# Kernel optimization log

Measured on AMD Instinct MI355X. Metric: run time of the kernel, lower is better.

## Reference

```python
import jax, jax.numpy as jnp
import numpy as np

B, N, DIN, DOUT = 32, 1024, 256, 256


def setup_inputs() -> dict:
    key = jax.random.key(0)
    ks = jax.random.split(key, 7)
    s = 1.0 / np.sqrt(DIN)
    return {
        "x": jax.random.normal(ks[0], (B, N, DIN), dtype=jnp.float32),
        "Wq": jax.random.uniform(ks[1], (DOUT, DIN), minval=-s, maxval=s, dtype=jnp.float32),
        "bq": jax.random.uniform(ks[2], (DOUT,), minval=-s, maxval=s, dtype=jnp.float32),
        "Wk": jax.random.uniform(ks[3], (DOUT, DIN), minval=-s, maxval=s, dtype=jnp.float32),
        "bk": jax.random.uniform(ks[4], (DOUT,), minval=-s, maxval=s, dtype=jnp.float32),
        "Wv": jax.random.uniform(ks[5], (DOUT, DIN), minval=-s, maxval=s, dtype=jnp.float32),
        "bv": jax.random.uniform(ks[6], (DOUT,), minval=-s, maxval=s, dtype=jnp.float32),
    }


def reference(x, Wq, bq, Wk, bk, Wv, bv):
    # q, k, v: (B, N, Dout)
    q = jnp.einsum("bnd,od->bno", x, Wq) + bq
    k = jnp.einsum("bnd,od->bno", x, Wk) + bk
    v = jnp.einsum("bnd,od->bno", x, Wv) + bv
    # logits: (B, N, N) = q @ k^T per batch
    logits = jnp.einsum("bnd,bmd->bnm", q, k)
    # NOTE: softmax over the BATCH dim (axis=0), as in the original module
    attn = jax.nn.softmax(logits, axis=0)
    out = jnp.einsum("bnm,bmd->bnd", attn, v)  # (B, N, Dout)
    return out
```

## Files before the change

### kernel.cpp

```cpp
#include <hip/hip_runtime.h>

typedef __bf16 bf16x8 __attribute__((ext_vector_type(8)));
typedef __bf16 bf16x4 __attribute__((ext_vector_type(4)));
typedef float  f32x4  __attribute__((ext_vector_type(4)));

#define BM 128
#define BN 128
#define BK 64

__device__ __forceinline__ void g2l16(const void* g, void* l) {
    __builtin_amdgcn_global_load_lds((const __attribute__((address_space(1))) void*)g,
                                     (__attribute__((address_space(3))) void*)l, 16, 0, 0);
}

template<int EPI>
__global__ __launch_bounds__(256)
void gemm_nt(const __bf16* __restrict__ A, const __bf16* __restrict__ B,
             void* __restrict__ Cv, const float* __restrict__ bias,
             int lda, int ldb, int ldc, int K,
             long sA, long sB, long sC)
{
    __shared__ __align__(16) char smem[36864];
    __bf16* As = (__bf16*)smem;
    __bf16* Bs = (__bf16*)(smem + 16384);

    const int tid  = threadIdx.x;
    const int w    = tid >> 6;
    const int lane = tid & 63;
    const int quad = lane >> 4;
    const int l16  = lane & 15;
    const int wm   = w & 1;
    const int wn   = w >> 1;

    const int m0 = blockIdx.x * BM;
    const int n0 = blockIdx.y * BN;
    const int z  = blockIdx.z;

    const __bf16* Ab = A + (size_t)z * sA;
    const __bf16* Bb = B + (size_t)z * sB;

    const int srow = (w << 3) + (lane >> 3);
    const int scol = ((lane & 7) ^ (lane >> 3)) << 3;
    char* ldsA = (char*)As + (size_t)w * 1024;
    char* ldsB = (char*)Bs + (size_t)w * 1024;

    const __bf16* Ag = Ab + (size_t)(m0 + srow) * lda + scol;
    const __bf16* Bg = Bb + (size_t)(n0 + srow) * ldb + scol;

    f32x4 acc[4][4] = {};

    for (int k0 = 0; k0 < K; k0 += BK) {
        __syncthreads();
        #pragma unroll
        for (int c = 0; c < 4; c++)
            g2l16(Ag + (size_t)(c * 32) * lda + k0, ldsA + c * 4096);
        #pragma unroll
        for (int c = 0; c < 4; c++)
            g2l16(Bg + (size_t)(c * 32) * ldb + k0, ldsB + c * 4096);
        __syncthreads();

        #pragma unroll
        for (int kk = 0; kk < BK; kk += 32) {
            const int ub = kk >> 3;
            bf16x8 a[4], b[4];
            #pragma unroll
            for (int mt = 0; mt < 4; mt++) {
                const int row = wm * 64 + mt * 16 + l16;
                const int cp  = ((quad + ub) ^ (row & 7)) << 3;
                a[mt] = *(const bf16x8*)&As[row * BK + cp];
            }
            #pragma unroll
            for (int nt = 0; nt < 4; nt++) {
                const int row = wn * 64 + nt * 16 + l16;
                const int cp  = ((quad + ub) ^ (row & 7)) << 3;
                b[nt] = *(const bf16x8*)&Bs[row * BK + cp];
            }
            #pragma unroll
            for (int mt = 0; mt < 4; mt++)
                #pragma unroll
                for (int nt = 0; nt < 4; nt++)
                    acc[mt][nt] = __builtin_amdgcn_mfma_f32_16x16x32_bf16(
                        a[mt], b[nt], acc[mt][nt], 0, 0, 0);
        }
    }

    __syncthreads();

    if constexpr (EPI == 2 || EPI == 4) {
        __bf16* eb = (__bf16*)smem;
        const bool tr = (EPI == 4) && (z == 2);
        if (!tr) {
            float bn[4];
            if constexpr (EPI == 4) {
                #pragma unroll
                for (int nt = 0; nt < 4; nt++)
                    bn[nt] = bias[z * 256 + n0 + wn * 64 + nt * 16 + l16];
            }
            #pragma unroll
            for (int mt = 0; mt < 4; mt++) {
                const int row = wm * 64 + mt * 16 + quad * 4;
                #pragma unroll
                for (int nt = 0; nt < 4; nt++) {
                    const int col = wn * 64 + nt * 16 + l16;
                    #pragma unroll
                    for (int r = 0; r < 4; r++) {
                        float v = acc[mt][nt][r];
                        if constexpr (EPI == 2) v = __expf(v);
                        else                    v += bn[nt];
                        eb[(row + r) * 144 + col] = (__bf16)v;
                    }
                }
            }
        } else {
            #pragma unroll
            for (int nt = 0; nt < 4; nt++) {
                const float bn = bias[z * 256 + n0 + wn * 64 + nt * 16 + l16];
                const int erow = wn * 64 + nt * 16 + l16;
                #pragma unroll
                for (int mt = 0; mt < 4; mt++) {
                    bf16x4 pk;
                    #pragma unroll
                    for (int r = 0; r < 4; r++) pk[r] = (__bf16)(acc[mt][nt][r] + bn);
                    *(bf16x4*)&eb[erow * 144 + wm * 64 + mt * 16 + quad * 4] = pk;
                }
            }
        }
        __syncthreads();
        const int row = tid >> 1, seg = tid & 1;
        __bf16* dst;
        if (!tr) {
            dst = (__bf16*)Cv + (size_t)z * sC + (size_t)(m0 + row) * ldc + n0 + seg * 64;
        } else {
            dst = (__bf16*)Cv + 2 * sC + (size_t)(m0 >> 10) * 262144
                + (size_t)(n0 + row) * 1024 + (m0 & 1023) + seg * 64;
        }
        #pragma unroll
        for (int u = 0; u < 8; u++)
            *(bf16x8*)(dst + u * 8) = *(const bf16x8*)&eb[row * 144 + seg * 64 + u * 8];
    } else {
        float* ef = (float*)smem;
        float* C  = (float*)Cv + (size_t)z * sC;
        #pragma unroll
        for (int h = 0; h < 2; h++) {
            if (h) __syncthreads();
            if (wm == h) {
                #pragma unroll
                for (int mt = 0; mt < 4; mt++) {
                    const int row = mt * 16 + quad * 4;
                    #pragma unroll
                    for (int nt = 0; nt < 4; nt++) {
                        const int col = wn * 64 + nt * 16 + l16;
                        #pragma unroll
                        for (int r = 0; r < 4; r++)
                            ef[(row + r) * 132 + col] = acc[mt][nt][r];
                    }
                }
            }
            __syncthreads();
            const int row = tid >> 2, seg = tid & 3;
            float* dst = C + (size_t)(m0 + h * 64 + row) * ldc + n0 + seg * 32;
            #pragma unroll
            for (int u = 0; u < 8; u++)
                *(f32x4*)(dst + u * 4) = *(const f32x4*)&ef[row * 132 + seg * 32 + u * 4];
        }
    }
}

__global__ __launch_bounds__(256)
void cvt_all(const float* __restrict__ x,
             const float* __restrict__ Wq, const float* __restrict__ Wk,
             const float* __restrict__ Wv,
             const float* __restrict__ bq, const float* __restrict__ bk,
             const float* __restrict__ bv,
             __bf16* __restrict__ xb, __bf16* __restrict__ Wqb,
             float* __restrict__ bpack)
{
    const int i = blockIdx.x * 256 + threadIdx.x;
    if (i < 1073152) {
        const float* s; __bf16* d; int off;
        if (i < 1048576)      { s = x;  d = xb;            off = i; }
        else if (i < 1056768) { s = Wq; d = Wqb;           off = i - 1048576; }
        else if (i < 1064960) { s = Wk; d = Wqb + 131072;  off = i - 1056768; }
        else                  { s = Wv; d = Wqb + 262144;  off = i - 1064960; }
        const float4* s4 = (const float4*)s;
        const float4 f0 = s4[off * 2], f1 = s4[off * 2 + 1];
        bf16x8 o;
        o[0] = (__bf16)f0.x; o[1] = (__bf16)f0.y; o[2] = (__bf16)f0.z; o[3] = (__bf16)f0.w;
        o[4] = (__bf16)f1.x; o[5] = (__bf16)f1.y; o[6] = (__bf16)f1.z; o[7] = (__bf16)f1.w;
        ((bf16x8*)d)[off] = o;
    } else if (i < 1073344) {
        const int j = i - 1073152;
        const int sel = j >> 6, jj = j & 63;
        const float* s = sel == 0 ? bq : (sel == 1 ? bk : bv);
        ((float4*)bpack)[j] = ((const float4*)s)[jj];
    }
}

__global__ __launch_bounds__(256)
void softmax_norm(__bf16* __restrict__ E)
{
    const size_t p = (size_t)blockIdx.x * 256 + threadIdx.x;
    bf16x8* E8 = (bf16x8*)E;
    bf16x8 e[32];
    #pragma unroll
    for (int b = 0; b < 32; b++) e[b] = E8[(size_t)b * 131072 + p];
    float s[8] = {0.f, 0.f, 0.f, 0.f, 0.f, 0.f, 0.f, 0.f};
    #pragma unroll
    for (int b = 0; b < 32; b++)
        #pragma unroll
        for (int j = 0; j < 8; j++) s[j] += (float)e[b][j];
    float rs[8];
    #pragma unroll
    for (int j = 0; j < 8; j++) rs[j] = 1.0f / s[j];
    #pragma unroll
    for (int b = 0; b < 32; b++) {
        bf16x8 o = e[b];
        #pragma unroll
        for (int j = 0; j < 8; j++) o[j] = (__bf16)((float)o[j] * rs[j]);
        E8[(size_t)b * 131072 + p] = o;
    }
}

extern "C" void kernel_launch(void* const* d_in, const int* in_sizes, int n_in,
                              void* d_out, int out_size, void* d_ws, size_t ws_size,
                              hipStream_t stream)
{
    const float* x  = (const float*)d_in[0];
    const float* Wq = (const float*)d_in[1];
    const float* bq = (const float*)d_in[2];
    const float* Wk = (const float*)d_in[3];
    const float* bk = (const float*)d_in[4];
    const float* Wv = (const float*)d_in[5];
    const float* bv = (const float*)d_in[6];
    float* out = (float*)d_out;

    char* ws = (char*)d_ws;
    __bf16* xb    = (__bf16*)(ws);
    __bf16* qkv   = (__bf16*)(ws + (16u << 20));
    __bf16* E     = (__bf16*)(ws + (64u << 20));
    __bf16* Wqb   = (__bf16*)(ws + (128u << 20));
    float*  bpack = (float*) (ws + (128u << 20) + (3u << 18));

    cvt_all<<<4194, 256, 0, stream>>>(x, Wq, Wk, Wv, bq, bk, bv, xb, Wqb, bpack);

    gemm_nt<4><<<dim3(256, 2, 3), 256, 0, stream>>>(xb, Wqb, qkv, bpack,
                                                    256, 256, 256, 256,
                                                    0, 131072, 8388608);

    gemm_nt<2><<<dim3(8, 8, 32), 256, 0, stream>>>(qkv, qkv + 8388608, E, nullptr,
                                                   256, 256, 1024, 256,
                                                   262144, 262144, 1048576);

    softmax_norm<<<512, 256, 0, stream>>>(E);

    gemm_nt<3><<<dim3(8, 2, 32), 256, 0, stream>>>(E, qkv + 2 * 8388608, out, nullptr,
                                                   1024, 1024, 256, 1024,
                                                   1048576, 262144, 262144);
}
```

Measured before the change: 232.8 us.

## Fuse softmax normalization into PV GEMM A-load and flatten batch-major grid

The softmax pass no longer rewrites E. It only computes per-position reciprocal sums over the batch and stores them as fp32. A new PV GEMM scales E by those reciprocals while staging the A tile into LDS, so one full read-write pass over the 64MB E buffer is gone. The QK GEMM now uses a flat grid with batch as the fastest index, so the 32 batches of the same tile run together, which may help the later cross-batch reduction hit L2. Epilogues now write registers straight to global memory instead of going through LDS, which risks less-coalesced stores. The PV A-tile is also loaded with plain register loads instead of async LDS loads, and it reads extra fp32 scale data.

Result: faster. 213.5 us (-8.3%).

```diff
diff --git a/kernel.cpp b/kernel.cpp
--- a/kernel.cpp
+++ b/kernel.cpp
@@ -13,16 +13,15 @@
                                      (__attribute__((address_space(3))) void*)l, 16, 0, 0);
 }
 
-template<int EPI>
+template<int EPI, int FLAT>
 __global__ __launch_bounds__(256)
 void gemm_nt(const __bf16* __restrict__ A, const __bf16* __restrict__ B,
              void* __restrict__ Cv, const float* __restrict__ bias,
              int lda, int ldb, int ldc, int K,
              long sA, long sB, long sC)
 {
-    __shared__ __align__(16) char smem[36864];
-    __bf16* As = (__bf16*)smem;
-    __bf16* Bs = (__bf16*)(smem + 16384);
+    __shared__ __align__(16) __bf16 As[BM * BK];
+    __shared__ __align__(16) __bf16 Bs[BN * BK];
 
     const int tid  = threadIdx.x;
     const int w    = tid >> 6;
@@ -32,9 +31,18 @@
     const int wm   = w & 1;
     const int wn   = w >> 1;
 
-    const int m0 = blockIdx.x * BM;
-    const int n0 = blockIdx.y * BN;
-    const int z  = blockIdx.z;
+    int m0, n0, z;
+    if constexpr (FLAT) {
+        const int id = blockIdx.x;
+        z = id & 31;
+        const int xy = id >> 5;
+        m0 = (xy & 7) * BM;
+        n0 = (xy >> 3) * BN;
+    } else {
+        m0 = blockIdx.x * BM;
+        n0 = blockIdx.y * BN;
+        z  = blockIdx.z;
+    }
 
     const __bf16* Ab = A + (size_t)z * sA;
     const __bf16* Bb = B + (size_t)z * sB;
@@ -84,84 +92,134 @@
         }
     }
 
-    __syncthreads();
-
-    if constexpr (EPI == 2 || EPI == 4) {
-        __bf16* eb = (__bf16*)smem;
-        const bool tr = (EPI == 4) && (z == 2);
-        if (!tr) {
-            float bn[4];
-            if constexpr (EPI == 4) {
+    #pragma unroll
+    for (int mt = 0; mt < 4; mt++) {
+        const int mb = m0 + wm * 64 + mt * 16 + quad * 4;
+        #pragma unroll
+        for (int nt = 0; nt < 4; nt++) {
+            const int n = n0 + wn * 64 + nt * 16 + l16;
+            if constexpr (EPI == 2) {
+                __bf16* C = (__bf16*)Cv + (size_t)z * sC;
                 #pragma unroll
-                for (int nt = 0; nt < 4; nt++)
-                    bn[nt] = bias[z * 256 + n0 + wn * 64 + nt * 16 + l16];
-            }
-            #pragma unroll
-            for (int mt = 0; mt < 4; mt++) {
-                const int row = wm * 64 + mt * 16 + quad * 4;
-                #pragma unroll
-                for (int nt = 0; nt < 4; nt++) {
-                    const int col = wn * 64 + nt * 16 + l16;
+                for (int r = 0; r < 4; r++)
+                    C[(size_t)(mb + r) * ldc + n] = (__bf16)__expf(acc[mt][nt][r]);
+            } else {
+                const float bn = bias[z * 256 + n];
+                if (z < 2) {
+                    __bf16* C = (__bf16*)Cv + (size_t)z * sC;
                     #pragma unroll
-                    for (int r = 0; r < 4; r++) {
-                        float v = acc[mt][nt][r];
-                        if constexpr (EPI == 2) v = __expf(v);
-                        else                    v += bn[nt];
-                        eb[(row + r) * 144 + col] = (__bf16)v;
-                    }
-                }
-            }
-        } else {
-            #pragma unroll
-            for (int nt = 0; nt < 4; nt++) {
-                const float bn = bias[z * 256 + n0 + wn * 64 + nt * 16 + l16];
-                const int erow = wn * 64 + nt * 16 + l16;
-                #pragma unroll
-                for (int mt = 0; mt < 4; mt++) {
+                    for (int r = 0; r < 4; r++)
+                        C[(size_t)(mb + r) * ldc + n] = (__bf16)(acc[mt][nt][r] + bn);
+                } else {
+                    __bf16* C = (__bf16*)Cv + 2 * sC;
+                    const int bidx = mb >> 10, mloc = mb & 1023;
                     bf16x4 pk;
                     #pragma unroll
                     for (int r = 0; r < 4; r++) pk[r] = (__bf16)(acc[mt][nt][r] + bn);
-                    *(bf16x4*)&eb[erow * 144 + wm * 64 + mt * 16 + quad * 4] = pk;
+                    *(bf16x4*)(C + (size_t)bidx * 262144 + (size_t)n * 1024 + mloc) = pk;
                 }
             }
         }
+    }
+}
+
+__global__ __launch_bounds__(256)
+void gemm_pv(const __bf16* __restrict__ E, const float* __restrict__ Srcp,
+             const __bf16* __restrict__ vT, float* __restrict__ out)
+{
+    __shared__ __align__(16) __bf16 As[128 * 64];
+    __shared__ __align__(16) __bf16 Bs[128 * 64];
+
+    const int tid  = threadIdx.x;
+    const int w    = tid >> 6;
+    const int lane = tid & 63;
+    const int quad = lane >> 4;
+    const int l16  = lane & 15;
+    const int wm   = w & 1;
+    const int wn   = w >> 1;
+
+    const int id = blockIdx.x;
+    const int z  = id & 31;
+    const int xy = id >> 5;
+    const int m0 = (xy & 7) * 128;
+    const int n0 = (xy >> 3) * 128;
+
+    const __bf16* Eb = E  + (size_t)z * 1048576;
+    const __bf16* Vb = vT + (size_t)z * 262144;
+    float*        Ob = out + (size_t)z * 262144;
+
+    const int srow = (w << 3) + (lane >> 3);
+    const int scol = ((lane & 7) ^ (lane >> 3)) << 3;
+    char* ldsB = (char*)Bs + (size_t)w * 1024;
+    const __bf16* Bg = Vb + (size_t)(n0 + srow) * 1024 + scol;
+
+    const int arow = tid >> 1;
+    const int auh  = (tid & 1) * 4;
+    const __bf16* Ag = Eb + (size_t)(m0 + arow) * 1024;
+    const float*  Sg = Srcp + (size_t)(m0 + arow) * 1024;
+    __bf16* Ad = As + arow * 64;
+
+    f32x4 acc[4][4] = {};
+
+    for (int k0 = 0; k0 < 1024; k0 += BK) {
         __syncthreads();
-        const int row = tid >> 1, seg = tid & 1;
-        __bf16* dst;
-        if (!tr) {
-            dst = (__bf16*)Cv + (size_t)z * sC + (size_t)(m0 + row) * ldc + n0 + seg * 64;
-        } else {
-            dst = (__bf16*)Cv + 2 * sC + (size_t)(m0 >> 10) * 262144
-                + (size_t)(n0 + row) * 1024 + (m0 & 1023) + seg * 64;
-        }
-        #pragma unroll
-        for (int u = 0; u < 8; u++)
-            *(bf16x8*)(dst + u * 8) = *(const bf16x8*)&eb[row * 144 + seg * 64 + u * 8];
-    } else {
-        float* ef = (float*)smem;
-        float* C  = (float*)Cv + (size_t)z * sC;
-        #pragma unroll
-        for (int h = 0; h < 2; h++) {
-            if (h) __syncthreads();
-            if (wm == h) {
+        #pragma unroll
+        for (int c = 0; c < 4; c++)
+            g2l16(Bg + (size_t)(c * 32) * 1024 + k0, ldsB + c * 4096);
+        #pragma unroll
+        for (int s = 0; s < 4; s++) {
+            const int u   = auh + s;
+            const int col = k0 + u * 8;
+            bf16x8 e  = *(const bf16x8*)(Ag + col);
+            f32x4  r0 = *(const f32x4*)(Sg + col);
+            f32x4  r1 = *(const f32x4*)(Sg + col + 4);
+            bf16x8 en;
+            en[0] = (__bf16)((float)e[0] * r0[0]);
+            en[1] = (__bf16)((float)e[1] * r0[1]);
+            en[2] = (__bf16)((float)e[2] * r0[2]);
+            en[3] = (__bf16)((float)e[3] * r0[3]);
+            en[4] = (__bf16)((float)e[4] * r1[0]);
+            en[5] = (__bf16)((float)e[5] * r1[1]);
+            en[6] = (__bf16)((float)e[6] * r1[2]);
+            en[7] = (__bf16)((float)e[7] * r1[3]);
+            *(bf16x8*)(Ad + ((u ^ (arow & 7)) << 3)) = en;
+        }
+        __syncthreads();
+
+        #pragma unroll
+        for (int kk = 0; kk < BK; kk += 32) {
+            const int ub = kk >> 3;
+            bf16x8 a[4], b[4];
+            #pragma unroll
+            for (int mt = 0; mt < 4; mt++) {
+                const int row = wm * 64 + mt * 16 + l16;
+                const int cp  = ((quad + ub) ^ (row & 7)) << 3;
+                a[mt] = *(const bf16x8*)&As[row * BK + cp];
+            }
+            #pragma unroll
+            for (int nt = 0; nt < 4; nt++) {
+                const int row = wn * 64 + nt * 16 + l16;
+                const int cp  = ((quad + ub) ^ (row & 7)) << 3;
+                b[nt] = *(const bf16x8*)&Bs[row * BK + cp];
+            }
+            #pragma unroll
+            for (int mt = 0; mt < 4; mt++)
                 #pragma unroll
-                for (int mt = 0; mt < 4; mt++) {
-                    const int row = mt * 16 + quad * 4;
-                    #pragma unroll
-                    for (int nt = 0; nt < 4; nt++) {
-                        const int col = wn * 64 + nt * 16 + l16;
-                        #pragma unroll
-                        for (int r = 0; r < 4; r++)
-                            ef[(row + r) * 132 + col] = acc[mt][nt][r];
-                    }
-                }
-            }
-            __syncthreads();
-            const int row = tid >> 2, seg = tid & 3;
-            float* dst = C + (size_t)(m0 + h * 64 + row) * ldc + n0 + seg * 32;
-            #pragma unroll
-            for (int u = 0; u < 8; u++)
-                *(f32x4*)(dst + u * 4) = *(const f32x4*)&ef[row * 132 + seg * 32 + u * 4];
+                for (int nt = 0; nt < 4; nt++)
+                    acc[mt][nt] = __builtin_amdgcn_mfma_f32_16x16x32_bf16(
+                        a[mt], b[nt], acc[mt][nt], 0, 0, 0);
+        }
+    }
+
+    #pragma unroll
+    for (int mt = 0; mt < 4; mt++) {
+        const int mb = m0 + wm * 64 + mt * 16 + quad * 4;
+        #pragma unroll
+        for (int nt = 0; nt < 4; nt++) {
+            const int n = n0 + wn * 64 + nt * 16 + l16;
+            #pragma unroll
+            for (int r = 0; r < 4; r++)
+                Ob[(size_t)(mb + r) * 256 + n] = acc[mt][nt][r];
         }
     }
 }
@@ -197,28 +255,24 @@
 }
 
 __global__ __launch_bounds__(256)
-void softmax_norm(__bf16* __restrict__ E)
+void reduce_s(const __bf16* __restrict__ E, float* __restrict__ Srcp)
 {
     const size_t p = (size_t)blockIdx.x * 256 + threadIdx.x;
-    bf16x8* E8 = (bf16x8*)E;
-    bf16x8 e[32];
-    #pragma unroll
-    for (int b = 0; b < 32; b++) e[b] = E8[(size_t)b * 131072 + p];
+    const bf16x8* E8 = (const bf16x8*)E;
     float s[8] = {0.f, 0.f, 0.f, 0.f, 0.f, 0.f, 0.f, 0.f};
     #pragma unroll
-    for (int b = 0; b < 32; b++)
-        #pragma unroll
-        for (int j = 0; j < 8; j++) s[j] += (float)e[b][j];
-    float rs[8];
-    #pragma unroll
-    for (int j = 0; j < 8; j++) rs[j] = 1.0f / s[j];
-    #pragma unroll
     for (int b = 0; b < 32; b++) {
-        bf16x8 o = e[b];
-        #pragma unroll
-        for (int j = 0; j < 8; j++) o[j] = (__bf16)((float)o[j] * rs[j]);
-        E8[(size_t)b * 131072 + p] = o;
-    }
+        bf16x8 e = E8[(size_t)b * 131072 + p];
+        #pragma unroll
+        for (int j = 0; j < 8; j++) s[j] += (float)e[j];
+    }
+    f32x4 r0, r1;
+    #pragma unroll
+    for (int j = 0; j < 4; j++) r0[j] = __builtin_amdgcn_rcpf(s[j]);
+    #pragma unroll
+    for (int j = 0; j < 4; j++) r1[j] = __builtin_amdgcn_rcpf(s[j + 4]);
+    ((f32x4*)Srcp)[p * 2]     = r0;
+    ((f32x4*)Srcp)[p * 2 + 1] = r1;
 }
 
 extern "C" void kernel_launch(void* const* d_in, const int* in_sizes, int n_in,
@@ -235,6 +289,7 @@
     float* out = (float*)d_out;
 
     char* ws = (char*)d_ws;
+    float*  Srcp  = (float*) (ws);
     __bf16* xb    = (__bf16*)(ws);
     __bf16* qkv   = (__bf16*)(ws + (16u << 20));
     __bf16* E     = (__bf16*)(ws + (64u << 20));
@@ -243,17 +298,15 @@
 
     cvt_all<<<4194, 256, 0, stream>>>(x, Wq, Wk, Wv, bq, bk, bv, xb, Wqb, bpack);
 
-    gemm_nt<4><<<dim3(256, 2, 3), 256, 0, stream>>>(xb, Wqb, qkv, bpack,
-                                                    256, 256, 256, 256,
-                                                    0, 131072, 8388608);
-
-    gemm_nt<2><<<dim3(8, 8, 32), 256, 0, stream>>>(qkv, qkv + 8388608, E, nullptr,
-                                                   256, 256, 1024, 256,
-                                                   262144, 262144, 1048576);
-
-    softmax_norm<<<512, 256, 0, stream>>>(E);
-
-    gemm_nt<3><<<dim3(8, 2, 32), 256, 0, stream>>>(E, qkv + 2 * 8388608, out, nullptr,
-                                                   1024, 1024, 256, 1024,
-                                                   1048576, 262144, 262144);
-}
+    gemm_nt<4, 0><<<dim3(256, 2, 3), 256, 0, stream>>>(xb, Wqb, qkv, bpack,
+                                                       256, 256, 256, 256,
+                                                       0, 131072, 8388608);
+
+    gemm_nt<2, 1><<<2048, 256, 0, stream>>>(qkv, qkv + 8388608, E, nullptr,
+                                            256, 256, 1024, 256,
+                                            262144, 262144, 1048576);
+
+    reduce_s<<<512, 256, 0, stream>>>(E, Srcp);
+
+    gemm_pv<<<512, 256, 0, stream>>>(E, Srcp, qkv + 2 * 8388608, out);
+}
```

## Split GEMM into specialized kernels with transposed tiles, direct epilogue stores, batch-interleaved grid

Applied to the files above, without the earlier changes.

Replaces the templated GEMM with three specialized kernels that share a core loop. Each kernel computes transposed output tiles (e.g. W·xᵀ, k·qᵀ), so the MFMA accumulator layout maps to contiguous 4-element stores, and the LDS staging epilogue and its extra barriers are dropped. V is written into a new vT layout with the batch interleaved, which lets the PV GEMM run as 64x128 tiles and doubles its block count. Block indices are remapped so adjacent blocks handle different batches, which may spread memory traffic. The direct stores are narrower (8 bytes for bf16) than the previous 16-byte coalesced stores, which risks lower store efficiency. The softmax reciprocal also switches to the hardware rcp.

Result: faster. 203.8 us (-12.4%).

```diff
diff --git a/kernel.cpp b/kernel.cpp
--- a/kernel.cpp
+++ b/kernel.cpp
@@ -4,164 +4,181 @@
 typedef __bf16 bf16x4 __attribute__((ext_vector_type(4)));
 typedef float  f32x4  __attribute__((ext_vector_type(4)));
 
-#define BM 128
-#define BN 128
-#define BK 64
-
 __device__ __forceinline__ void g2l16(const void* g, void* l) {
     __builtin_amdgcn_global_load_lds((const __attribute__((address_space(1))) void*)g,
                                      (__attribute__((address_space(3))) void*)l, 16, 0, 0);
 }
 
-template<int EPI>
-__global__ __launch_bounds__(256)
-void gemm_nt(const __bf16* __restrict__ A, const __bf16* __restrict__ B,
-             void* __restrict__ Cv, const float* __restrict__ bias,
-             int lda, int ldb, int ldc, int K,
-             long sA, long sB, long sC)
-{
-    __shared__ __align__(16) char smem[36864];
-    __bf16* As = (__bf16*)smem;
-    __bf16* Bs = (__bf16*)(smem + 16384);
-
-    const int tid  = threadIdx.x;
-    const int w    = tid >> 6;
-    const int lane = tid & 63;
-    const int quad = lane >> 4;
-    const int l16  = lane & 15;
-    const int wm   = w & 1;
-    const int wn   = w >> 1;
-
-    const int m0 = blockIdx.x * BM;
-    const int n0 = blockIdx.y * BN;
-    const int z  = blockIdx.z;
-
-    const __bf16* Ab = A + (size_t)z * sA;
-    const __bf16* Bb = B + (size_t)z * sB;
+template<int MCH, int NCH>
+__device__ __forceinline__ void gemm_core(
+    const __bf16* __restrict__ At, const __bf16* __restrict__ Bt,
+    int lda, int ldb, int K,
+    __bf16* As, __bf16* Bs, f32x4 (&acc)[MCH][NCH], int tid)
+{
+    const int w = tid >> 6, lane = tid & 63;
+    const int quad = lane >> 4, l16 = lane & 15;
+    const int wm = w & 1, wn = w >> 1;
 
     const int srow = (w << 3) + (lane >> 3);
     const int scol = ((lane & 7) ^ (lane >> 3)) << 3;
     char* ldsA = (char*)As + (size_t)w * 1024;
     char* ldsB = (char*)Bs + (size_t)w * 1024;
-
-    const __bf16* Ag = Ab + (size_t)(m0 + srow) * lda + scol;
-    const __bf16* Bg = Bb + (size_t)(n0 + srow) * ldb + scol;
-
-    f32x4 acc[4][4] = {};
-
-    for (int k0 = 0; k0 < K; k0 += BK) {
+    const __bf16* Ag = At + (size_t)srow * lda + scol;
+    const __bf16* Bg = Bt + (size_t)srow * ldb + scol;
+
+    for (int k0 = 0; k0 < K; k0 += 64) {
         __syncthreads();
         #pragma unroll
-        for (int c = 0; c < 4; c++)
+        for (int c = 0; c < MCH; c++)
             g2l16(Ag + (size_t)(c * 32) * lda + k0, ldsA + c * 4096);
         #pragma unroll
-        for (int c = 0; c < 4; c++)
+        for (int c = 0; c < NCH; c++)
             g2l16(Bg + (size_t)(c * 32) * ldb + k0, ldsB + c * 4096);
         __syncthreads();
 
         #pragma unroll
-        for (int kk = 0; kk < BK; kk += 32) {
+        for (int kk = 0; kk < 64; kk += 32) {
             const int ub = kk >> 3;
-            bf16x8 a[4], b[4];
-            #pragma unroll
-            for (int mt = 0; mt < 4; mt++) {
-                const int row = wm * 64 + mt * 16 + l16;
-                const int cp  = ((quad + ub) ^ (row & 7)) << 3;
-                a[mt] = *(const bf16x8*)&As[row * BK + cp];
+            bf16x8 a[MCH], b[NCH];
+            #pragma unroll
+            for (int mt = 0; mt < MCH; mt++) {
+                const int row = wm * (MCH * 16) + mt * 16 + l16;
+                a[mt] = *(const bf16x8*)&As[row * 64 + (((quad + ub) ^ (row & 7)) << 3)];
             }
             #pragma unroll
-            for (int nt = 0; nt < 4; nt++) {
-                const int row = wn * 64 + nt * 16 + l16;
-                const int cp  = ((quad + ub) ^ (row & 7)) << 3;
-                b[nt] = *(const bf16x8*)&Bs[row * BK + cp];
+            for (int nt = 0; nt < NCH; nt++) {
+                const int row = wn * (NCH * 16) + nt * 16 + l16;
+                b[nt] = *(const bf16x8*)&Bs[row * 64 + (((quad + ub) ^ (row & 7)) << 3)];
             }
             #pragma unroll
-            for (int mt = 0; mt < 4; mt++)
+            for (int mt = 0; mt < MCH; mt++)
                 #pragma unroll
-                for (int nt = 0; nt < 4; nt++)
+                for (int nt = 0; nt < NCH; nt++)
                     acc[mt][nt] = __builtin_amdgcn_mfma_f32_16x16x32_bf16(
                         a[mt], b[nt], acc[mt][nt], 0, 0, 0);
         }
     }
-
-    __syncthreads();
-
-    if constexpr (EPI == 2 || EPI == 4) {
-        __bf16* eb = (__bf16*)smem;
-        const bool tr = (EPI == 4) && (z == 2);
-        if (!tr) {
-            float bn[4];
-            if constexpr (EPI == 4) {
+}
+
+
+__global__ __launch_bounds__(256)
+void gemm_proj(const __bf16* __restrict__ xb, const __bf16* __restrict__ Wb,
+               const float* __restrict__ bpack, __bf16* __restrict__ qkv,
+               __bf16* __restrict__ vT)
+{
+    __shared__ __align__(16) __bf16 As[128 * 64];
+    __shared__ __align__(16) __bf16 Bs[128 * 64];
+    const int tid = threadIdx.x;
+    const int id  = blockIdx.x;
+    const int z   = id >> 9;
+    const int rr  = id & 511;
+
+    const __bf16 *At, *Bt;
+    int m0, n0;
+    if (z < 2) {
+        m0 = (rr & 1) * 128; n0 = (rr >> 1) * 128;
+        At = Wb + z * 131072 + m0 * 256;
+        Bt = xb + (size_t)n0 * 256;
+    } else {
+        m0 = (rr >> 1) * 128; n0 = (rr & 1) * 128;
+        At = xb + (size_t)m0 * 256;
+        Bt = Wb + 2 * 131072 + n0 * 256;
+    }
+
+    f32x4 acc[4][4] = {};
+    gemm_core<4, 4>(At, Bt, 256, 256, 256, As, Bs, acc, tid);
+
+    const int w = tid >> 6, lane = tid & 63, quad = lane >> 4, l16 = lane & 15;
+    const int wm = w & 1, wn = w >> 1;
+    #pragma unroll
+    for (int mt = 0; mt < 4; mt++) {
+        const int i0 = m0 + wm * 64 + mt * 16 + quad * 4;
+        #pragma unroll
+        for (int nt = 0; nt < 4; nt++) {
+            const int j = n0 + wn * 64 + nt * 16 + l16;
+            bf16x4 pk;
+            if (z < 2) {
+                const f32x4 bn = *(const f32x4*)&bpack[z * 256 + i0];
                 #pragma unroll
-                for (int nt = 0; nt < 4; nt++)
-                    bn[nt] = bias[z * 256 + n0 + wn * 64 + nt * 16 + l16];
+                for (int r = 0; r < 4; r++) pk[r] = (__bf16)(acc[mt][nt][r] + bn[r]);
+                *(bf16x4*)(qkv + (size_t)z * 8388608 + (size_t)j * 256 + i0) = pk;
+            } else {
+                const float bn = bpack[512 + j];
+                #pragma unroll
+                for (int r = 0; r < 4; r++) pk[r] = (__bf16)(acc[mt][nt][r] + bn);
+                *(bf16x4*)(vT + (size_t)j * 32768 + i0) = pk;
             }
-            #pragma unroll
-            for (int mt = 0; mt < 4; mt++) {
-                const int row = wm * 64 + mt * 16 + quad * 4;
-                #pragma unroll
-                for (int nt = 0; nt < 4; nt++) {
-                    const int col = wn * 64 + nt * 16 + l16;
-                    #pragma unroll
-                    for (int r = 0; r < 4; r++) {
-                        float v = acc[mt][nt][r];
-                        if constexpr (EPI == 2) v = __expf(v);
-                        else                    v += bn[nt];
-                        eb[(row + r) * 144 + col] = (__bf16)v;
-                    }
-                }
-            }
-        } else {
-            #pragma unroll
-            for (int nt = 0; nt < 4; nt++) {
-                const float bn = bias[z * 256 + n0 + wn * 64 + nt * 16 + l16];
-                const int erow = wn * 64 + nt * 16 + l16;
-                #pragma unroll
-                for (int mt = 0; mt < 4; mt++) {
-                    bf16x4 pk;
-                    #pragma unroll
-                    for (int r = 0; r < 4; r++) pk[r] = (__bf16)(acc[mt][nt][r] + bn);
-                    *(bf16x4*)&eb[erow * 144 + wm * 64 + mt * 16 + quad * 4] = pk;
-                }
-            }
-        }
-        __syncthreads();
-        const int row = tid >> 1, seg = tid & 1;
-        __bf16* dst;
-        if (!tr) {
-            dst = (__bf16*)Cv + (size_t)z * sC + (size_t)(m0 + row) * ldc + n0 + seg * 64;
-        } else {
-            dst = (__bf16*)Cv + 2 * sC + (size_t)(m0 >> 10) * 262144
-                + (size_t)(n0 + row) * 1024 + (m0 & 1023) + seg * 64;
-        }
-        #pragma unroll
-        for (int u = 0; u < 8; u++)
-            *(bf16x8*)(dst + u * 8) = *(const bf16x8*)&eb[row * 144 + seg * 64 + u * 8];
-    } else {
-        float* ef = (float*)smem;
-        float* C  = (float*)Cv + (size_t)z * sC;
-        #pragma unroll
-        for (int h = 0; h < 2; h++) {
-            if (h) __syncthreads();
-            if (wm == h) {
-                #pragma unroll
-                for (int mt = 0; mt < 4; mt++) {
-                    const int row = mt * 16 + quad * 4;
-                    #pragma unroll
-                    for (int nt = 0; nt < 4; nt++) {
-                        const int col = wn * 64 + nt * 16 + l16;
-                        #pragma unroll
-                        for (int r = 0; r < 4; r++)
-                            ef[(row + r) * 132 + col] = acc[mt][nt][r];
-                    }
-                }
-            }
-            __syncthreads();
-            const int row = tid >> 2, seg = tid & 3;
-            float* dst = C + (size_t)(m0 + h * 64 + row) * ldc + n0 + seg * 32;
-            #pragma unroll
-            for (int u = 0; u < 8; u++)
-                *(f32x4*)(dst + u * 4) = *(const f32x4*)&ef[row * 132 + seg * 32 + u * 4];
+        }
+    }
+}
+
+__global__ __launch_bounds__(256)
+void gemm_logits(const __bf16* __restrict__ qb, const __bf16* __restrict__ kb,
+                 __bf16* __restrict__ E)
+{
+    __shared__ __align__(16) __bf16 As[128 * 64];
+    __shared__ __align__(16) __bf16 Bs[128 * 64];
+    const int tid = threadIdx.x;
+    const int id  = blockIdx.x;
+    const int x = id & 7, s = id >> 3;
+    const int z = x + ((s >> 6) << 3);
+    const int t = s & 63;
+    const int m0 = (t & 7) * 128;
+    const int n0 = (t >> 3) * 128;
+
+    const __bf16* At = kb + (size_t)z * 262144 + m0 * 256;
+    const __bf16* Bt = qb + (size_t)z * 262144 + n0 * 256;
+
+    f32x4 acc[4][4] = {};
+    gemm_core<4, 4>(At, Bt, 256, 256, 256, As, Bs, acc, tid);
+
+    const int w = tid >> 6, lane = tid & 63, quad = lane >> 4, l16 = lane & 15;
+    const int wm = w & 1, wn = w >> 1;
+    __bf16* Eb = E + (size_t)z * 1048576;
+    #pragma unroll
+    for (int mt = 0; mt < 4; mt++) {
+        const int i0 = m0 + wm * 64 + mt * 16 + quad * 4;
+        #pragma unroll
+        for (int nt = 0; nt < 4; nt++) {
+            const int j = n0 + wn * 64 + nt * 16 + l16;
+            bf16x4 pk;
+            #pragma unroll
+            for (int r = 0; r < 4; r++) pk[r] = (__bf16)__expf(acc[mt][nt][r]);
+            *(bf16x4*)(Eb + (size_t)j * 1024 + i0) = pk;
+        }
+    }
+}
+
+__global__ __launch_bounds__(256)
+void gemm_pv(const __bf16* __restrict__ vT, const __bf16* __restrict__ E,
+             float* __restrict__ out)
+{
+    __shared__ __align__(16) __bf16 As[64 * 64];
+    __shared__ __align__(16) __bf16 Bs[128 * 64];
+    const int tid = threadIdx.x;
+    const int id  = blockIdx.x;
+    const int x = id & 7, s = id >> 3;
+    const int z = x + ((s >> 5) << 3);
+    const int t = s & 31;
+    const int m0 = (t & 3) * 64;
+    const int n0 = (t >> 2) * 128;
+
+    const __bf16* At = vT + (size_t)m0 * 32768 + z * 1024;
+    const __bf16* Bt = E + (size_t)z * 1048576 + (size_t)n0 * 1024;
+
+    f32x4 acc[2][4] = {};
+    gemm_core<2, 4>(At, Bt, 32768, 1024, 1024, As, Bs, acc, tid);
+
+    const int w = tid >> 6, lane = tid & 63, quad = lane >> 4, l16 = lane & 15;
+    const int wm = w & 1, wn = w >> 1;
+    float* Ob = out + (size_t)z * 262144;
+    #pragma unroll
+    for (int mt = 0; mt < 2; mt++) {
+        const int i0 = m0 + wm * 32 + mt * 16 + quad * 4;
+        #pragma unroll
+        for (int nt = 0; nt < 4; nt++) {
+            const int j = n0 + wn * 64 + nt * 16 + l16;
+            *(f32x4*)(Ob + (size_t)j * 256 + i0) = acc[mt][nt];
         }
     }
 }
@@ -211,7 +228,7 @@
         for (int j = 0; j < 8; j++) s[j] += (float)e[b][j];
     float rs[8];
     #pragma unroll
-    for (int j = 0; j < 8; j++) rs[j] = 1.0f / s[j];
+    for (int j = 0; j < 8; j++) rs[j] = __builtin_amdgcn_rcpf(s[j]);
     #pragma unroll
     for (int b = 0; b < 32; b++) {
         bf16x8 o = e[b];
@@ -237,23 +254,18 @@
     char* ws = (char*)d_ws;
     __bf16* xb    = (__bf16*)(ws);
     __bf16* qkv   = (__bf16*)(ws + (16u << 20));
+    __bf16* vT    = (__bf16*)(ws + (48u << 20));
     __bf16* E     = (__bf16*)(ws + (64u << 20));
     __bf16* Wqb   = (__bf16*)(ws + (128u << 20));
     float*  bpack = (float*) (ws + (128u << 20) + (3u << 18));
 
     cvt_all<<<4194, 256, 0, stream>>>(x, Wq, Wk, Wv, bq, bk, bv, xb, Wqb, bpack);
 
-    gemm_nt<4><<<dim3(256, 2, 3), 256, 0, stream>>>(xb, Wqb, qkv, bpack,
-                                                    256, 256, 256, 256,
-                                                    0, 131072, 8388608);
-
-    gemm_nt<2><<<dim3(8, 8, 32), 256, 0, stream>>>(qkv, qkv + 8388608, E, nullptr,
-                                                   256, 256, 1024, 256,
-                                                   262144, 262144, 1048576);
+    gemm_proj<<<1536, 256, 0, stream>>>(xb, Wqb, bpack, qkv, vT);
+
+    gemm_logits<<<2048, 256, 0, stream>>>(qkv, qkv + 8388608, E);
 
     softmax_norm<<<512, 256, 0, stream>>>(E);
 
-    gemm_nt<3><<<dim3(8, 2, 32), 256, 0, stream>>>(E, qkv + 2 * 8388608, out, nullptr,
-                                                   1024, 1024, 256, 1024,
-                                                   1048576, 262144, 262144);
-}
+    gemm_pv<<<1024, 256, 0, stream>>>(vT, E, out);
+}
```
